# Kernel optimization log

Hardware: AMD Instinct MI355X
Metric: run time of the kernel (lower is better)

The kernel has to match this reference:

```python
import jax, jax.numpy as jnp
import numpy as np

B, C, H, W = 8, 256, 32, 32
N_HEAD, D_K, D_V, OUT_C = 8, 32, 32, 256


def _relative_indices(height, width):
    # idx[i, j] = (y_j - y_i + H) * W + (x_j - x_i + W), matching the torch loop
    ys, xs = np.meshgrid(np.arange(height), np.arange(width), indexing='ij')
    ys, xs = ys.reshape(-1), xs.reshape(-1)  # [L]
    rel_y = ys[None, :] - ys[:, None] + height  # [L, L]
    rel_x = xs[None, :] - xs[:, None] + width
    return jnp.asarray(rel_y * width + rel_x, dtype=jnp.int32)


def setup_inputs() -> dict:
    key = jax.random.key(0)
    ks = jax.random.split(key, 7)
    sc = lambda fan_in: 1.0 / np.sqrt(fan_in)
    table = ((2 * H - 1) * (2 * W - 1))  # 3969
    return {
        'x': jax.random.normal(ks[0], (B, C, H, W), jnp.float32),
        'Qw': jax.random.normal(ks[1], (C, N_HEAD * D_K), jnp.float32) * sc(C),
        'Kw': jax.random.normal(ks[2], (C, N_HEAD * D_K), jnp.float32) * sc(C),
        'Vw': jax.random.normal(ks[3], (C, N_HEAD * D_V), jnp.float32) * sc(C),
        'ffw': jax.random.normal(ks[4], (N_HEAD * D_V, OUT_C), jnp.float32) * sc(N_HEAD * D_V),
        'ffb': jax.random.normal(ks[5], (OUT_C,), jnp.float32) * 0.01,
        'rel_bias': jax.random.normal(ks[6], (N_HEAD, table), jnp.float32),
        'rel_idx': _relative_indices(H, W),  # [L, L] int32
    }


def reference(x, Qw, Kw, Vw, ffw, ffb, rel_bias, rel_idx):
    b, c, h_, w_ = x.shape
    L = h_ * w_
    nh = rel_bias.shape[0]
    dk = Qw.shape[1] // nh
    dv = Vw.shape[1] // nh
    xf = x.reshape(b, c, L).transpose(0, 2, 1)  # [b, L, c]
    q = (xf @ Qw).reshape(b, L, nh, dk).transpose(0, 2, 1, 3)  # [b, h, L, dk]
    k = (xf @ Kw).reshape(b, L, nh, dk).transpose(0, 2, 1, 3)
    v = (xf @ Vw).reshape(b, L, nh, dv).transpose(0, 2, 1, 3)
    bias = rel_bias[:, rel_idx]  # gather -> [h, L, L]
    sim = jnp.einsum('bhid,bhjd->bhij', q, k) + bias[None]  # no 1/sqrt(dk) in original
    attn = jax.nn.softmax(sim, axis=-1)  # dropout is identity in eval
    out = jnp.einsum('bhij,bhjd->bhid', attn, v)  # [b, h, L, dv]
    out = out.transpose(0, 2, 1, 3).reshape(b, L, nh * dv)
    out = out @ ffw + ffb  # [b, L, out_c]
    return out.transpose(0, 2, 1).reshape(b, -1, h_, w_)
```

## Files before the change

kernel.cpp:

```cpp
#include <hip/hip_runtime.h>
#include <math.h>


typedef unsigned short u16;
typedef __bf16 bf16;
typedef bf16 bf16x8 __attribute__((ext_vector_type(8)));
typedef bf16 bf16x4 __attribute__((ext_vector_type(4)));
typedef short s16x4 __attribute__((ext_vector_type(4)));
typedef float f32x4 __attribute__((ext_vector_type(4)));
typedef float f32x4u __attribute__((ext_vector_type(4), aligned(4)));
typedef u16 u16x8 __attribute__((ext_vector_type(8)));
typedef u16 u16x4 __attribute__((ext_vector_type(4)));

#define DEVI __device__ __forceinline__

DEVI u16 bfbits(float f) { return __builtin_bit_cast(u16, (bf16)f); }

DEVI void async_cp16(const u16* g, u16* l) {
    __builtin_amdgcn_global_load_lds((const __attribute__((address_space(1))) void*)g,
                                     (__attribute__((address_space(3))) void*)l, 16, 0, 0);
}

DEVI f32x4 pv_mfma(bf16x4 a, bf16x4 b, f32x4 c) {
#if __has_builtin(__builtin_amdgcn_mfma_f32_16x16x16bf16_1k)
    return __builtin_amdgcn_mfma_f32_16x16x16bf16_1k(
        __builtin_bit_cast(s16x4, a), __builtin_bit_cast(s16x4, b), c, 0, 0, 0);
#else
    asm("s_nop 1\n\tv_mfma_f32_16x16x16_bf16 %0, %1, %2, %0"
        : "+v"(c) : "v"(a), "v"(b));
    return c;
#endif
}

__global__ __launch_bounds__(256) void prep(const float* __restrict__ X,
                                            const float* __restrict__ Qw, const float* __restrict__ Kw,
                                            const float* __restrict__ Vw, const float* __restrict__ Fw,
                                            const float* __restrict__ RB,
                                            u16* __restrict__ XF, u16* __restrict__ WT,
                                            float* __restrict__ RBs) {
    __shared__ u16 t[64 * 65];
    const int blk = blockIdx.x, tid = threadIdx.x;
    if (blk < 576) {
        const float* src;
        int cbase, rbase, rows_total;
        u16* dst;
        if (blk < 512) {
            const int b = blk >> 6;
            cbase = (blk & 3) * 64; rbase = ((blk >> 2) & 15) * 64;
            src = X + (size_t)b * 256 * 1024; dst = XF + (size_t)b * 1024 * 256;
            rows_total = 1024;
        } else {
            const int t2 = blk - 512, wsel = t2 >> 4;
            cbase = (t2 & 3) * 64; rbase = ((t2 >> 2) & 3) * 64;
            src = wsel == 0 ? Qw : wsel == 1 ? Kw : wsel == 2 ? Vw : Fw;
            dst = WT + (size_t)wsel * 256 * 256;
            rows_total = 256;
        }
        const int w = tid >> 6, r = tid & 63;
#pragma unroll
        for (int i = 0; i < 16; i++) {
            const int c = w * 16 + i;
            t[c * 65 + r] = bfbits(src[(size_t)(cbase + c) * rows_total + rbase + r]);
        }
        __syncthreads();
#pragma unroll
        for (int i = 0; i < 2; i++) {
            const int idx = i * 256 + tid;
            const int r2 = idx >> 3, cg = idx & 7;
            u16x8 v;
#pragma unroll
            for (int j = 0; j < 8; j++) v[j] = t[(cg * 8 + j) * 65 + r2];
            *(u16x8*)&dst[(size_t)(rbase + r2) * 256 + cbase + cg * 8] = v;
        }
    } else {
        const int n = 8 * 3969;
        for (int i = (blk - 576) * 256 + tid; i < n; i += 32 * 256)
            RBs[i] = RB[i] * 1.44269504f;
    }
}

template <int MFR, int PASS>
__global__ __launch_bounds__(256, 3) void gemm_fused(const u16* __restrict__ xf, const u16* __restrict__ wt,
                                                     u16* __restrict__ q, u16* __restrict__ kk,
                                                     u16* __restrict__ vt, const u16* __restrict__ ob,
                                                     float* __restrict__ outf, const float* __restrict__ ffb) {
    constexpr int TM = MFR * 32;
    __shared__ __align__(16) u16 lA[2][TM * 32];
    __shared__ __align__(16) u16 lB[2][64 * 32];
    const int tid = threadIdx.x;
    const int wave = tid >> 6, lane = tid & 63;
    const int quad = lane >> 4, l15 = lane & 15;

    int mode, mbase, nbase;
    const u16 *A, *Bt;
    if (PASS == 2) {
        mode = 2; A = wt + 768 * 256; Bt = ob;
        mbase = (blockIdx.x & 3) * 64; nbase = (blockIdx.x >> 2) * 64;
    } else if (blockIdx.x < 512) {
        mode = 0; A = xf; Bt = wt;
        mbase = (blockIdx.x >> 3) * TM; nbase = (blockIdx.x & 7) * 64;
    } else {
        mode = 1; A = wt + 512 * 256; Bt = xf;
        const int t = blockIdx.x - 512;
        mbase = (t & 1) * TM; nbase = (t >> 1) * 64;
    }

    const int m0 = (wave >> 1) * (MFR * 16), n0 = (wave & 1) * 32;
    const int srow = tid >> 2;
    const int sgcol = (lane & 3) ^ ((lane >> 3) & 3);
    const int kcol = ((quad ^ ((l15 >> 1) & 3))) * 8;

    f32x4 acc[MFR][2];
#pragma unroll
    for (int i = 0; i < MFR; i++)
#pragma unroll
        for (int j = 0; j < 2; j++) acc[i][j] = f32x4{0.f, 0.f, 0.f, 0.f};

#pragma unroll
    for (int half = 0; half < MFR / 2; half++)
        async_cp16(&A[(size_t)(mbase + half * 64 + srow) * 256 + sgcol * 8],
                   &lA[0][half * 2048 + wave * 512]);
    async_cp16(&Bt[(size_t)(nbase + srow) * 256 + sgcol * 8], &lB[0][wave * 512]);
    __syncthreads();

#pragma unroll
    for (int t = 0; t < 8; ++t) {
        const int cur = t & 1;
        if (t < 7) {
            const int kb = (t + 1) * 32;
#pragma unroll
            for (int half = 0; half < MFR / 2; half++)
                async_cp16(&A[(size_t)(mbase + half * 64 + srow) * 256 + kb + sgcol * 8],
                           &lA[cur ^ 1][half * 2048 + wave * 512]);
            async_cp16(&Bt[(size_t)(nbase + srow) * 256 + kb + sgcol * 8], &lB[cur ^ 1][wave * 512]);
        }
        bf16x8 af[MFR], bfr[2];
#pragma unroll
        for (int i = 0; i < MFR; i++) af[i] = *(const bf16x8*)&lA[cur][(m0 + i * 16 + l15) * 32 + kcol];
#pragma unroll
        for (int j = 0; j < 2; j++) bfr[j] = *(const bf16x8*)&lB[cur][(n0 + j * 16 + l15) * 32 + kcol];
#pragma unroll
        for (int i = 0; i < MFR; i++)
#pragma unroll
            for (int j = 0; j < 2; j++)
                acc[i][j] = __builtin_amdgcn_mfma_f32_16x16x32_bf16(af[i], bfr[j], acc[i][j], 0, 0, 0);
        __syncthreads();
    }

#pragma unroll
    for (int i = 0; i < MFR; i++) {
#pragma unroll
        for (int j = 0; j < 2; j++) {
#pragma unroll
            for (int r = 0; r < 4; r++) {
                const int gm = mbase + m0 + i * 16 + quad * 4 + r;
                const int gn = nbase + n0 + j * 16 + l15;
                float v = acc[i][j][r];
                if (mode == 0) {
                    const int b = gm >> 10, l = gm & 1023;
                    int n = gn;
                    u16* dst = q;
                    if (n >= 256) { n -= 256; dst = kk; }
                    else v *= 1.44269504f;
                    const int h = n >> 5, d = n & 31;
                    dst[(((size_t)(b * 8 + h) * 1024 + l) << 5) + d] = bfbits(v);
                } else if (mode == 1) {
                    const int h = gm >> 5, d = gm & 31;
                    const int b = gn >> 10, l = gn & 1023;
                    vt[(((size_t)(b * 8 + h) * 32 + d) << 10) + l] = bfbits(v);
                } else {
                    const int b = gn >> 10, l = gn & 1023;
                    outf[(((size_t)(b * 256 + gm)) << 10) + l] = v + ffb[gm];
                }
            }
        }
    }
}

__global__ __launch_bounds__(256, 2) void attn(const u16* __restrict__ Q, const u16* __restrict__ Kb,
                                               const u16* __restrict__ Vt, const float* __restrict__ RBs,
                                               u16* __restrict__ O) {
    __shared__ __align__(16) u16 kbuf[2][32 * 32];
    __shared__ __align__(16) u16 vbuf[2][32 * 32];
    const int tid = threadIdx.x;
    const int wave = tid >> 6, lane = tid & 63;
    const int quad = lane >> 4, l15 = lane & 15;
    const int blk = blockIdx.x;
    const int bh = ((blk >> 6) << 3) + (blk & 7);
    const int qt = (blk >> 3) & 7;
    const int b = bh >> 3, h = bh & 7;
    const int qbase = qt * 128 + wave * 32;
    const size_t bhL = (size_t)bh * 1024;

    const bf16x8 qfA = *(const bf16x8*)&Q[(bhL + qbase + l15) * 32 + quad * 8];
    const bf16x8 qfB = *(const bf16x8*)&Q[(bhL + qbase + 16 + l15) * 32 + quad * 8];
    const float* brow0 = RBs + (size_t)h * 3969
                         + (32 - (qbase >> 5)) * 32 + 32 - l15 + quad * 4;
    const int srow = lane >> 2;
    const int sgcol = (lane & 3) ^ ((lane >> 3) & 3);
    const u16* ksrc = &Kb[bhL * 32];
    const u16* vsrc_lo = &Vt[(((size_t)bh * 32) + srow) << 10];
    const u16* vsrc_hi = &Vt[(((size_t)bh * 32) + 16 + srow) << 10];

    f32x4 oA_lo{0.f, 0.f, 0.f, 0.f}, oA_hi{0.f, 0.f, 0.f, 0.f};
    f32x4 oB_lo{0.f, 0.f, 0.f, 0.f}, oB_hi{0.f, 0.f, 0.f, 0.f};
    f32x4 sacA{0.f, 0.f, 0.f, 0.f}, sacB{0.f, 0.f, 0.f, 0.f};
    const bf16 one1 = (bf16)1.f;
    const bf16x4 onesb = {one1, one1, one1, one1};

    const int swz = (l15 >> 1) & 3;
    const int kcol = (quad ^ swz) * 8;
    const int g0 = (2 * ((quad >> 1) ^ swz) + (quad & 1)) * 4;
    const int g1 = (2 * (((quad >> 1) + 2) ^ swz) + (quad & 1)) * 4;

    f32x4u bmA, b0A, b1A, bmB, b0B, b1B;

#define BLOADA(c) do {                                          \
        bmA = *(const f32x4u*)(brow0 + (c) * 32 - 16);          \
        b0A = *(const f32x4u*)(brow0 + (c) * 32);               \
        b1A = *(const f32x4u*)(brow0 + (c) * 32 + 16);          \
    } while (0)
#define BLOADB(c) do {                                          \
        bmB = *(const f32x4u*)(brow0 + (c) * 32 - 16);          \
        b0B = *(const f32x4u*)(brow0 + (c) * 32);               \
        b1B = *(const f32x4u*)(brow0 + (c) * 32 + 16);          \
    } while (0)

#define STAGE(buf, c) do {                                                                   \
        const int kb_ = (c) * 32;                                                            \
        if (wave == 0)                                                                       \
            async_cp16(ksrc + kb_ * 32 + srow * 32 + sgcol * 8, &kbuf[buf][0]);              \
        else if (wave == 1)                                                                  \
            async_cp16(ksrc + kb_ * 32 + 512 + srow * 32 + sgcol * 8, &kbuf[buf][512]);      \
        else if (wave == 2)                                                                  \
            async_cp16(vsrc_lo + kb_ + sgcol * 8, &vbuf[buf][0]);                            \
        else                                                                                 \
            async_cp16(vsrc_hi + kb_ + sgcol * 8, &vbuf[buf][512]);                          \
    } while (0)

#define COMPUTE(cur, BM, B0, B1) do {                                                     \
        const bf16x8 kf0 = *(const bf16x8*)&kbuf[cur][l15 * 32 + kcol];                   \
        const bf16x8 kf1 = *(const bf16x8*)&kbuf[cur][(16 + l15) * 32 + kcol];            \
        const bf16x4 v00 = __builtin_bit_cast(bf16x4, *(const u16x4*)&vbuf[cur][l15 * 32 + g0]); \
        const bf16x4 v10 = __builtin_bit_cast(bf16x4, *(const u16x4*)&vbuf[cur][l15 * 32 + g1]); \
        const bf16x4 v01 = __builtin_bit_cast(bf16x4, *(const u16x4*)&vbuf[cur][(16 + l15) * 32 + g0]); \
        const bf16x4 v11 = __builtin_bit_cast(bf16x4, *(const u16x4*)&vbuf[cur][(16 + l15) * 32 + g1]); \
        f32x4 s0A = __builtin_amdgcn_mfma_f32_16x16x32_bf16(kf0, qfA, __builtin_bit_cast(f32x4, (B0)), 0, 0, 0); \
        f32x4 s1A = __builtin_amdgcn_mfma_f32_16x16x32_bf16(kf1, qfA, __builtin_bit_cast(f32x4, (B1)), 0, 0, 0); \
        f32x4 s0B = __builtin_amdgcn_mfma_f32_16x16x32_bf16(kf0, qfB, __builtin_bit_cast(f32x4, (BM)), 0, 0, 0); \
        f32x4 s1B = __builtin_amdgcn_mfma_f32_16x16x32_bf16(kf1, qfB, __builtin_bit_cast(f32x4, (B0)), 0, 0, 0); \
        bf16x4 p0A, p1A, p0B, p1B;                                                        \
        _Pragma("unroll")                                                                 \
        for (int r = 0; r < 4; r++) {                                                     \
            p0A[r] = (bf16)__builtin_amdgcn_exp2f(s0A[r]);                                \
            p1A[r] = (bf16)__builtin_amdgcn_exp2f(s1A[r]);                                \
            p0B[r] = (bf16)__builtin_amdgcn_exp2f(s0B[r]);                                \
            p1B[r] = (bf16)__builtin_amdgcn_exp2f(s1B[r]);                                \
        }                                                                                 \
        oA_lo = pv_mfma(p0A, v00, oA_lo);                                                 \
        oA_hi = pv_mfma(p0A, v01, oA_hi);                                                 \
        oA_lo = pv_mfma(p1A, v10, oA_lo);                                                 \
        oA_hi = pv_mfma(p1A, v11, oA_hi);                                                 \
        sacA = pv_mfma(p0A, onesb, sacA);                                                 \
        sacA = pv_mfma(p1A, onesb, sacA);                                                 \
        oB_lo = pv_mfma(p0B, v00, oB_lo);                                                 \
        oB_hi = pv_mfma(p0B, v01, oB_hi);                                                 \
        oB_lo = pv_mfma(p1B, v10, oB_lo);                                                 \
        oB_hi = pv_mfma(p1B, v11, oB_hi);                                                 \
        sacB = pv_mfma(p0B, onesb, sacB);                                                 \
        sacB = pv_mfma(p1B, onesb, sacB);                                                 \
    } while (0)

#define WAIT3 asm volatile("s_waitcnt vmcnt(3)" ::: "memory")
#define WAIT0 asm volatile("s_waitcnt vmcnt(0)" ::: "memory")
#define BAR __builtin_amdgcn_s_barrier()

    BLOADA(0); BLOADB(1);
    STAGE(0, 0);
    WAIT0; BAR;
    for (int c = 0; c < 30; c += 2) {
        STAGE(1, c + 1); COMPUTE(0, bmA, b0A, b1A); BLOADA(c + 2); WAIT3; BAR;
        STAGE(0, c + 2); COMPUTE(1, bmB, b0B, b1B); BLOADB(c + 3); WAIT3; BAR;
    }
    STAGE(1, 31); COMPUTE(0, bmA, b0A, b1A); WAIT0; BAR;
    COMPUTE(1, bmB, b0B, b1B);
#undef BLOADA
#undef BLOADB
#undef STAGE
#undef COMPUTE
#undef WAIT3
#undef WAIT0
#undef BAR

#pragma unroll
    for (int r = 0; r < 4; r++) {
        const float invA = 1.f / sacA[r];
        const float invB = 1.f / sacB[r];
        const int iA = qbase + quad * 4 + r;
        const int iB = iA + 16;
        O[((size_t)(b * 1024 + iA) * 256) + h * 32 + l15] = bfbits(oA_lo[r] * invA);
        O[((size_t)(b * 1024 + iA) * 256) + h * 32 + 16 + l15] = bfbits(oA_hi[r] * invA);
        O[((size_t)(b * 1024 + iB) * 256) + h * 32 + l15] = bfbits(oB_lo[r] * invB);
        O[((size_t)(b * 1024 + iB) * 256) + h * 32 + 16 + l15] = bfbits(oB_hi[r] * invB);
    }
}

extern "C" void kernel_launch(void* const* d_in, const int* in_sizes, int n_in,
                              void* d_out, int out_size, void* d_ws, size_t ws_size,
                              hipStream_t stream) {
    const float* x   = (const float*)d_in[0];
    const float* Qw  = (const float*)d_in[1];
    const float* Kw  = (const float*)d_in[2];
    const float* Vw  = (const float*)d_in[3];
    const float* Fw  = (const float*)d_in[4];
    const float* ffb = (const float*)d_in[5];
    const float* RB  = (const float*)d_in[6];

    u16* ws = (u16*)d_ws;
    u16* xf = ws;
    u16* wt = xf + 2097152;
    u16* q  = wt + 262144;
    u16* kk = q  + 2097152;
    u16* vt = kk + 2097152;
    float* RBs = (float*)(vt + 2097152);
    u16* ob = xf;

    prep<<<dim3(608), 256, 0, stream>>>(x, Qw, Kw, Vw, Fw, RB, xf, wt, RBs);
    gemm_fused<4, 0><<<dim3(768), 256, 0, stream>>>(xf, wt, q, kk, vt, nullptr, nullptr, nullptr);
    attn<<<dim3(512), 256, 0, stream>>>(q, kk, vt, RBs, ob);
    gemm_fused<2, 2><<<dim3(512), 256, 0, stream>>>(xf, wt, q, kk, vt, ob, (float*)d_out, ffb);
}
```

Baseline: 120.8 us.

## Load K/V fragments directly from global into registers, dropping LDS staging and barriers

```diff
diff --git a/kernel.cpp b/kernel.cpp
--- a/kernel.cpp
+++ b/kernel.cpp
@@ -180,8 +180,6 @@
 __global__ __launch_bounds__(256, 2) void attn(const u16* __restrict__ Q, const u16* __restrict__ Kb,
                                                const u16* __restrict__ Vt, const float* __restrict__ RBs,
                                                u16* __restrict__ O) {
-    __shared__ __align__(16) u16 kbuf[2][32 * 32];
-    __shared__ __align__(16) u16 vbuf[2][32 * 32];
     const int tid = threadIdx.x;
     const int wave = tid >> 6, lane = tid & 63;
     const int quad = lane >> 4, l15 = lane & 15;
@@ -196,11 +194,10 @@
     const bf16x8 qfB = *(const bf16x8*)&Q[(bhL + qbase + 16 + l15) * 32 + quad * 8];
     const float* brow0 = RBs + (size_t)h * 3969
                          + (32 - (qbase >> 5)) * 32 + 32 - l15 + quad * 4;
-    const int srow = lane >> 2;
-    const int sgcol = (lane & 3) ^ ((lane >> 3) & 3);
-    const u16* ksrc = &Kb[bhL * 32];
-    const u16* vsrc_lo = &Vt[(((size_t)bh * 32) + srow) << 10];
-    const u16* vsrc_hi = &Vt[(((size_t)bh * 32) + 16 + srow) << 10];
+    const u16* kr0 = &Kb[bhL * 32] + (size_t)l15 * 32 + quad * 8;
+    const u16* kr1 = kr0 + 16 * 32;
+    const u16* vr_lo = &Vt[((size_t)(bh * 32) + l15) << 10] + quad * 4;
+    const u16* vr_hi = vr_lo + (16 << 10);
 
     f32x4 oA_lo{0.f, 0.f, 0.f, 0.f}, oA_hi{0.f, 0.f, 0.f, 0.f};
     f32x4 oB_lo{0.f, 0.f, 0.f, 0.f}, oB_hi{0.f, 0.f, 0.f, 0.f};
@@ -208,47 +205,28 @@
     const bf16 one1 = (bf16)1.f;
     const bf16x4 onesb = {one1, one1, one1, one1};
 
-    const int swz = (l15 >> 1) & 3;
-    const int kcol = (quad ^ swz) * 8;
-    const int g0 = (2 * ((quad >> 1) ^ swz) + (quad & 1)) * 4;
-    const int g1 = (2 * (((quad >> 1) + 2) ^ swz) + (quad & 1)) * 4;
-
-    f32x4u bmA, b0A, b1A, bmB, b0B, b1B;
-
-#define BLOADA(c) do {                                          \
-        bmA = *(const f32x4u*)(brow0 + (c) * 32 - 16);          \
-        b0A = *(const f32x4u*)(brow0 + (c) * 32);               \
-        b1A = *(const f32x4u*)(brow0 + (c) * 32 + 16);          \
+    bf16x8 k0_0, k1_0, k0_1, k1_1;
+    bf16x4 va_0, vb_0, vc_0, vd_0, va_1, vb_1, vc_1, vd_1;
+    f32x4u bm_0, b0_0, b1_0, bm_1, b0_1, b1_1;
+
+#define LOADS(P, c) do {                                                        \
+        const int kb_ = (c) * 32;                                               \
+        k0_##P = *(const bf16x8*)(kr0 + (size_t)kb_ * 32);                      \
+        k1_##P = *(const bf16x8*)(kr1 + (size_t)kb_ * 32);                      \
+        va_##P = *(const bf16x4*)(vr_lo + kb_);                                 \
+        vb_##P = *(const bf16x4*)(vr_lo + kb_ + 16);                            \
+        vc_##P = *(const bf16x4*)(vr_hi + kb_);                                 \
+        vd_##P = *(const bf16x4*)(vr_hi + kb_ + 16);                            \
+        bm_##P = *(const f32x4u*)(brow0 + (c) * 32 - 16);                       \
+        b0_##P = *(const f32x4u*)(brow0 + (c) * 32);                            \
+        b1_##P = *(const f32x4u*)(brow0 + (c) * 32 + 16);                       \
     } while (0)
-#define BLOADB(c) do {                                          \
-        bmB = *(const f32x4u*)(brow0 + (c) * 32 - 16);          \
-        b0B = *(const f32x4u*)(brow0 + (c) * 32);               \
-        b1B = *(const f32x4u*)(brow0 + (c) * 32 + 16);          \
-    } while (0)
-
-#define STAGE(buf, c) do {                                                                   \
-        const int kb_ = (c) * 32;                                                            \
-        if (wave == 0)                                                                       \
-            async_cp16(ksrc + kb_ * 32 + srow * 32 + sgcol * 8, &kbuf[buf][0]);              \
-        else if (wave == 1)                                                                  \
-            async_cp16(ksrc + kb_ * 32 + 512 + srow * 32 + sgcol * 8, &kbuf[buf][512]);      \
-        else if (wave == 2)                                                                  \
-            async_cp16(vsrc_lo + kb_ + sgcol * 8, &vbuf[buf][0]);                            \
-        else                                                                                 \
-            async_cp16(vsrc_hi + kb_ + sgcol * 8, &vbuf[buf][512]);                          \
-    } while (0)
-
-#define COMPUTE(cur, BM, B0, B1) do {                                                     \
-        const bf16x8 kf0 = *(const bf16x8*)&kbuf[cur][l15 * 32 + kcol];                   \
-        const bf16x8 kf1 = *(const bf16x8*)&kbuf[cur][(16 + l15) * 32 + kcol];            \
-        const bf16x4 v00 = __builtin_bit_cast(bf16x4, *(const u16x4*)&vbuf[cur][l15 * 32 + g0]); \
-        const bf16x4 v10 = __builtin_bit_cast(bf16x4, *(const u16x4*)&vbuf[cur][l15 * 32 + g1]); \
-        const bf16x4 v01 = __builtin_bit_cast(bf16x4, *(const u16x4*)&vbuf[cur][(16 + l15) * 32 + g0]); \
-        const bf16x4 v11 = __builtin_bit_cast(bf16x4, *(const u16x4*)&vbuf[cur][(16 + l15) * 32 + g1]); \
-        f32x4 s0A = __builtin_amdgcn_mfma_f32_16x16x32_bf16(kf0, qfA, __builtin_bit_cast(f32x4, (B0)), 0, 0, 0); \
-        f32x4 s1A = __builtin_amdgcn_mfma_f32_16x16x32_bf16(kf1, qfA, __builtin_bit_cast(f32x4, (B1)), 0, 0, 0); \
-        f32x4 s0B = __builtin_amdgcn_mfma_f32_16x16x32_bf16(kf0, qfB, __builtin_bit_cast(f32x4, (BM)), 0, 0, 0); \
-        f32x4 s1B = __builtin_amdgcn_mfma_f32_16x16x32_bf16(kf1, qfB, __builtin_bit_cast(f32x4, (B0)), 0, 0, 0); \
+
+#define COMPUTE(P) do {                                                                   \
+        f32x4 s0A = __builtin_amdgcn_mfma_f32_16x16x32_bf16(k0_##P, qfA, __builtin_bit_cast(f32x4, b0_##P), 0, 0, 0); \
+        f32x4 s1A = __builtin_amdgcn_mfma_f32_16x16x32_bf16(k1_##P, qfA, __builtin_bit_cast(f32x4, b1_##P), 0, 0, 0); \
+        f32x4 s0B = __builtin_amdgcn_mfma_f32_16x16x32_bf16(k0_##P, qfB, __builtin_bit_cast(f32x4, bm_##P), 0, 0, 0); \
+        f32x4 s1B = __builtin_amdgcn_mfma_f32_16x16x32_bf16(k1_##P, qfB, __builtin_bit_cast(f32x4, b0_##P), 0, 0, 0); \
         bf16x4 p0A, p1A, p0B, p1B;                                                        \
         _Pragma("unroll")                                                                 \
         for (int r = 0; r < 4; r++) {                                                     \
@@ -257,40 +235,37 @@
             p0B[r] = (bf16)__builtin_amdgcn_exp2f(s0B[r]);                                \
             p1B[r] = (bf16)__builtin_amdgcn_exp2f(s1B[r]);                                \
         }                                                                                 \
-        oA_lo = pv_mfma(p0A, v00, oA_lo);                                                 \
-        oA_hi = pv_mfma(p0A, v01, oA_hi);                                                 \
-        oA_lo = pv_mfma(p1A, v10, oA_lo);                                                 \
-        oA_hi = pv_mfma(p1A, v11, oA_hi);                                                 \
+        oA_lo = pv_mfma(p0A, va_##P, oA_lo);                                              \
+        oA_hi = pv_mfma(p0A, vc_##P, oA_hi);                                              \
+        oA_lo = pv_mfma(p1A, vb_##P, oA_lo);                                              \
+        oA_hi = pv_mfma(p1A, vd_##P, oA_hi);                                              \
         sacA = pv_mfma(p0A, onesb, sacA);                                                 \
         sacA = pv_mfma(p1A, onesb, sacA);                                                 \
-        oB_lo = pv_mfma(p0B, v00, oB_lo);                                                 \
-        oB_hi = pv_mfma(p0B, v01, oB_hi);                                                 \
-        oB_lo = pv_mfma(p1B, v10, oB_lo);                                                 \
-        oB_hi = pv_mfma(p1B, v11, oB_hi);                                                 \
+        oB_lo = pv_mfma(p0B, va_##P, oB_lo);                                              \
+        oB_hi = pv_mfma(p0B, vc_##P, oB_hi);                                              \
+        oB_lo = pv_mfma(p1B, vb_##P, oB_lo);                                              \
+        oB_hi = pv_mfma(p1B, vd_##P, oB_hi);                                              \
         sacB = pv_mfma(p0B, onesb, sacB);                                                 \
         sacB = pv_mfma(p1B, onesb, sacB);                                                 \
     } while (0)
 
-#define WAIT3 asm volatile("s_waitcnt vmcnt(3)" ::: "memory")
+#define WAIT9 asm volatile("s_waitcnt vmcnt(9)" ::: "memory")
 #define WAIT0 asm volatile("s_waitcnt vmcnt(0)" ::: "memory")
-#define BAR __builtin_amdgcn_s_barrier()
-
-    BLOADA(0); BLOADB(1);
-    STAGE(0, 0);
-    WAIT0; BAR;
-    for (int c = 0; c < 30; c += 2) {
-        STAGE(1, c + 1); COMPUTE(0, bmA, b0A, b1A); BLOADA(c + 2); WAIT3; BAR;
-        STAGE(0, c + 2); COMPUTE(1, bmB, b0B, b1B); BLOADB(c + 3); WAIT3; BAR;
-    }
-    STAGE(1, 31); COMPUTE(0, bmA, b0A, b1A); WAIT0; BAR;
-    COMPUTE(1, bmB, b0B, b1B);
-#undef BLOADA
-#undef BLOADB
-#undef STAGE
+
+    LOADS(0, 0);
+    LOADS(1, 1);
+    for (int c = 0; c < 28; c += 2) {
+        WAIT9; COMPUTE(0); LOADS(0, c + 2);
+        WAIT9; COMPUTE(1); LOADS(1, c + 3);
+    }
+    WAIT9; COMPUTE(0); LOADS(0, 30);
+    WAIT9; COMPUTE(1); LOADS(1, 31);
+    WAIT9; COMPUTE(0);
+    WAIT0; COMPUTE(1);
+#undef LOADS
 #undef COMPUTE
-#undef WAIT3
+#undef WAIT9
 #undef WAIT0
-#undef BAR
 
 #pragma unroll
     for (int r = 0; r < 4; r++) {
```

New measurement: 140.5 us. 16.4% more time.
